# Performance work log

Measured on AMD Instinct MI355X. Metric: run time of the kernel, lower is better.

The kernel has to match this reference:

```python
import jax, jax.numpy as jnp
import numpy as np


def setup_inputs() -> dict:
    key = jax.random.key(0)
    k1, k2 = jax.random.split(key)
    z = jax.random.normal(k1, (16, 128, 32, 32), dtype=jnp.float32)
    e = jax.random.normal(k2, (8192, 128), dtype=jnp.float32)
    log_sigma = jnp.zeros((1,), dtype=jnp.float32)  # init_log_sigma = 0.0
    return {"z": z, "e": e, "log_sigma": log_sigma}


def reference(z, e, log_sigma):
    # z: [B, C, H, W] latents; e: [M, C] codebook; log_sigma: [1]
    B, C, H, W = z.shape
    zf = jnp.transpose(z, (0, 2, 3, 1)).reshape(-1, C)  # [N, C]
    N = zf.shape[0]
    M = e.shape[0]
    T = 1.0  # latent_temp default

    # squared L2 distance via expanded dot products: ||z||^2 + ||e||^2 - 2 z.e
    z_sq = jnp.sum(zf * zf, axis=1, keepdims=True)          # [N, 1]
    e_sq = jnp.sum(e * e, axis=1)[None, :]                  # [1, M]
    dist = jnp.maximum(z_sq + e_sq - 2.0 * (zf @ e.T), 0.0)  # [N, M]

    alpha = -1.0 / (2.0 * jnp.exp(log_sigma[0]) ** 2)
    A = alpha * dist / T                                     # [N, M]

    # np.log(np.e) == 1.0 in the original
    const = 0.5 * C * (2.0 * log_sigma - 1.0)                # [1]
    lse1_loss = -jnp.mean(T * jax.nn.logsumexp(A, axis=1)) + const + jnp.log(float(M))
    lse2_loss = -jnp.mean(T * jax.nn.logsumexp(A, axis=0)) + const + jnp.log(float(N))
    return lse1_loss, lse2_loss
```

## Files before the change

kernel.cpp:

```cpp
#include <hip/hip_runtime.h>
#include <hip/hip_bf16.h>

typedef unsigned short u16;
typedef __attribute__((ext_vector_type(8))) short short8;
typedef __attribute__((ext_vector_type(4))) float float4v;

#define N_ROWS 16384
#define M_COLS 8192
#define KDIM   128
#define SHIFT  64.0f
#define STRIPES 64
#define SPLITS  8
#define TILES   16

__device__ inline u16 f2bf(float f) {
  unsigned u = __builtin_bit_cast(unsigned, f);
  unsigned r = (u + 0x7fffu + ((u >> 16) & 1u)) >> 16;
  return (u16)r;
}

__global__ void prep(const float* __restrict__ z, const float* __restrict__ e,
                     u16* __restrict__ zf, u16* __restrict__ ef,
                     float* __restrict__ zsq, float* __restrict__ esq) {
  if (blockIdx.x < 512) {
    const int b = blockIdx.x >> 5, h = blockIdx.x & 31;
    __shared__ float tile[128 * 33];
    __shared__ float psum[8][32];
    const float* src = z + ((size_t)b * 128 * 32 + h) * 32;
    for (int idx = threadIdx.x; idx < 4096; idx += 256) {
      int c = idx >> 5, w = idx & 31;
      tile[c * 33 + w] = src[c * 1024 + w];
    }
    __syncthreads();
    {
      int w = threadIdx.x & 31, cg = threadIdx.x >> 5;
      float s = 0.f;
#pragma unroll
      for (int cc = 0; cc < 16; ++cc) {
        float v = tile[(cg * 16 + cc) * 33 + w];
        s = fmaf(v, v, s);
      }
      psum[cg][w] = s;
    }
    for (int idx = threadIdx.x; idx < 512; idx += 256) {
      int w = idx >> 4, g = idx & 15;
      short8 v;
#pragma unroll
      for (int cc = 0; cc < 8; ++cc) v[cc] = (short)f2bf(tile[(g * 8 + cc) * 33 + w]);
      *(short8*)&zf[((size_t)b * 1024 + h * 32 + w) * 128 + g * 8] = v;
    }
    __syncthreads();
    if (threadIdx.x < 32) {
      int w = threadIdx.x;
      float s = 0.f;
#pragma unroll
      for (int cg = 0; cg < 8; ++cg) s += psum[cg][w];
      zsq[b * 1024 + h * 32 + w] = s;
    }
  } else {
    const int gw = ((blockIdx.x - 512) * 256 + threadIdx.x) >> 6;
    const int ln = threadIdx.x & 63;
    for (int r = gw; r < M_COLS; r += 256) {
      float2 v = *(const float2*)&e[r * 128 + ln * 2];
      unsigned pk = (unsigned)f2bf(v.x) | ((unsigned)f2bf(v.y) << 16);
      *(unsigned*)&ef[r * 128 + ln * 2] = pk;
      float s = fmaf(v.x, v.x, v.y * v.y);
#pragma unroll
      for (int sh = 1; sh < 64; sh <<= 1) s += __shfl_xor(s, sh);
      if (ln == 0) esq[r] = s;
    }
  }
}

__global__ __launch_bounds__(256, 2) void gemm_lse(
    const u16* __restrict__ zf, const u16* __restrict__ ef,
    const float* __restrict__ zsq, const float* __restrict__ esq,
    const float* __restrict__ log_sigma,
    float* __restrict__ rpart, float* __restrict__ cpart) {
  __shared__ __align__(16) u16 et[2][64 * 128];
  __shared__ float colacc[1024];
  const int tid = threadIdx.x;
  const int ln = tid & 63, wv = tid >> 6;
  const int l15 = ln & 15, q = ln >> 4;
  const int stripe = blockIdx.x, split = blockIdx.y;
  const int colbase = split * 1024;

  for (int i = tid; i < 1024; i += 256) colacc[i] = 0.f;

  short8 af[4][4];
#pragma unroll
  for (int i = 0; i < 4; ++i)
#pragma unroll
    for (int kk = 0; kk < 4; ++kk)
      af[i][kk] = *(const short8*)(zf +
          (size_t)(stripe * 256 + wv * 64 + i * 16 + l15) * 128 + kk * 32 + q * 8);

  const float lsv = log_sigma[0];
  const float sg = __expf(lsv);
  const float alpha = -0.5f / (sg * sg);
  const float L2E = 1.44269504088896f;
  const float ca = alpha * L2E, cb = SHIFT * L2E, m2ca = -2.0f * ca;

  float4v zbl[4];
#pragma unroll
  for (int i = 0; i < 4; ++i) {
    float4v zs = *(const float4v*)(zsq + stripe * 256 + wv * 64 + i * 16 + q * 4);
#pragma unroll
    for (int r = 0; r < 4; ++r) zbl[i][r] = fmaf(ca, zs[r], cb);
  }

  float2 rs2[4][2];
#pragma unroll
  for (int i = 0; i < 4; ++i)
#pragma unroll
    for (int p = 0; p < 2; ++p) rs2[i][p] = make_float2(0.f, 0.f);

#define STAGE(tt)                                                              \
  do {                                                                         \
    const u16* efb = ef + (size_t)(colbase + (tt) * 64) * 128;                 \
    u16* dstb = et[(tt) & 1];                                                  \
    _Pragma("unroll")                                                          \
    for (int it = 0; it < 4; ++it) {                                           \
      int u = it * 256 + tid;                                                  \
      int r = u >> 4, p_ = u & 15;                                             \
      int g = p_ ^ (r & 15);                                                   \
      __builtin_amdgcn_global_load_lds(                                        \
          (const __attribute__((address_space(1))) unsigned int*)(efb + r * 128 + g * 8), \
          (__attribute__((address_space(3))) unsigned int*)(dstb + (it * 256 + wv * 64) * 8), \
          16, 0, 0);                                                           \
    }                                                                          \
  } while (0)

  STAGE(0);

  for (int t = 0; t < TILES; ++t) {
    __syncthreads();
    const u16* bb = et[t & 1];

    float4v acc[4][4];
#pragma unroll
    for (int kk = 0; kk < 4; ++kk) {
      short8 bfr[4];
      const int poff = ((kk * 4 + q) ^ l15) * 8;
#pragma unroll
      for (int j = 0; j < 4; ++j)
        bfr[j] = *(const short8*)(bb + (j * 16 + l15) * 128 + poff);
      if (kk == 0) {
#pragma unroll
        for (int i = 0; i < 4; ++i)
#pragma unroll
          for (int j = 0; j < 4; ++j)
            acc[i][j] = __builtin_amdgcn_mfma_f32_16x16x32_bf16(
                af[i][0], bfr[j], (float4v){0.f, 0.f, 0.f, 0.f}, 0, 0, 0);
      } else {
#pragma unroll
        for (int i = 0; i < 4; ++i)
#pragma unroll
          for (int j = 0; j < 4; ++j)
            acc[i][j] = __builtin_amdgcn_mfma_f32_16x16x32_bf16(
                af[i][kk], bfr[j], acc[i][j], 0, 0, 0);
      }
    }

    if (t + 1 < TILES) STAGE(t + 1);

    float ebv[4];
#pragma unroll
    for (int j = 0; j < 4; ++j) ebv[j] = ca * esq[colbase + t * 64 + j * 16 + l15];

    float2 cs2[4];
#pragma unroll
    for (int j = 0; j < 4; ++j) cs2[j] = make_float2(0.f, 0.f);

#pragma unroll
    for (int i = 0; i < 4; ++i) {
#pragma unroll
      for (int j = 0; j < 4; ++j) {
        float e0 = __builtin_amdgcn_exp2f(fmaf(acc[i][j][0], m2ca, zbl[i][0] + ebv[j]));
        float e1 = __builtin_amdgcn_exp2f(fmaf(acc[i][j][1], m2ca, zbl[i][1] + ebv[j]));
        float e2 = __builtin_amdgcn_exp2f(fmaf(acc[i][j][2], m2ca, zbl[i][2] + ebv[j]));
        float e3 = __builtin_amdgcn_exp2f(fmaf(acc[i][j][3], m2ca, zbl[i][3] + ebv[j]));
        rs2[i][0].x += e0; rs2[i][0].y += e1;
        rs2[i][1].x += e2; rs2[i][1].y += e3;
        cs2[j].x += e0 + e2; cs2[j].y += e1 + e3;
      }
    }
#pragma unroll
    for (int j = 0; j < 4; ++j) {
      float c = cs2[j].x + cs2[j].y;
      c += __shfl_xor(c, 16);
      c += __shfl_xor(c, 32);
      if (q == 0) atomicAdd(&colacc[t * 64 + j * 16 + l15], c);
    }
  }

  __syncthreads();
  for (int i = tid; i < 1024; i += 256)
    cpart[(size_t)stripe * 8192 + colbase + i] = colacc[i];

#pragma unroll
  for (int i = 0; i < 4; ++i)
#pragma unroll
    for (int p = 0; p < 2; ++p)
      for (int s = 1; s < 16; s <<= 1) {
        rs2[i][p].x += __shfl_xor(rs2[i][p].x, s);
        rs2[i][p].y += __shfl_xor(rs2[i][p].y, s);
      }
  if (l15 == 0) {
#pragma unroll
    for (int i = 0; i < 4; ++i) {
      int rbase = (size_t)0 + stripe * 256 + wv * 64 + i * 16 + q * 4;
      rpart[(size_t)split * N_ROWS + rbase + 0] = rs2[i][0].x;
      rpart[(size_t)split * N_ROWS + rbase + 1] = rs2[i][0].y;
      rpart[(size_t)split * N_ROWS + rbase + 2] = rs2[i][1].x;
      rpart[(size_t)split * N_ROWS + rbase + 3] = rs2[i][1].y;
    }
  }
#undef STAGE
}

__global__ void fin1(const float* __restrict__ rpart, const float* __restrict__ cpart,
                     double* __restrict__ lpart) {
  const int tid = threadIdx.x, b = blockIdx.x;
  double v;
  if (b < 64) {
    int row = b * 256 + tid;
    float s = 0.f;
#pragma unroll
    for (int p = 0; p < SPLITS; ++p) s += rpart[(size_t)p * N_ROWS + row];
    v = (double)logf(s);
  } else {
    int col = (b - 64) * 256 + tid;
    float s = 0.f;
#pragma unroll
    for (int p = 0; p < STRIPES; ++p) s += cpart[(size_t)p * M_COLS + col];
    v = (double)logf(s);
  }
  __shared__ double red[256];
  red[tid] = v;
  __syncthreads();
  for (int s = 128; s > 0; s >>= 1) {
    if (tid < s) red[tid] += red[tid + s];
    __syncthreads();
  }
  if (tid == 0) lpart[b] = red[0];
}

__global__ void fin2(const double* __restrict__ lpart,
                     const float* __restrict__ log_sigma, float* __restrict__ out) {
  const int tid = threadIdx.x;
  float lsv = log_sigma[0];
  float cst = 0.5f * 128.0f * (2.0f * lsv - 1.0f);
  if (tid == 0) {
    double s = 0.0;
    for (int i = 0; i < 64; ++i) s += lpart[i];
    out[0] = (float)(-(s / N_ROWS - (double)SHIFT)) + cst + logf((float)M_COLS);
  } else if (tid == 1) {
    double s = 0.0;
    for (int i = 64; i < 96; ++i) s += lpart[i];
    out[1] = (float)(-(s / M_COLS - (double)SHIFT)) + cst + logf((float)N_ROWS);
  }
}

extern "C" void kernel_launch(void* const* d_in, const int* in_sizes, int n_in,
                              void* d_out, int out_size, void* d_ws, size_t ws_size,
                              hipStream_t stream) {
  const float* z  = (const float*)d_in[0];
  const float* e  = (const float*)d_in[1];
  const float* ls = (const float*)d_in[2];
  float* out = (float*)d_out;
  char* ws = (char*)d_ws;
  u16*   zf    = (u16*)ws;
  u16*   ef    = (u16*)(ws + (4u << 20));
  float* zsq   = (float*)(ws + (6u << 20));
  float* esq   = (float*)(ws + (6u << 20) + (64u << 10));
  float* rpart = (float*)(ws + (6u << 20) + (96u << 10));
  float* cpart = (float*)(ws + (6u << 20) + (608u << 10));
  double* lpart = (double*)(ws + (6u << 20) + (608u << 10) + (2u << 20));

  prep<<<dim3(576), dim3(256), 0, stream>>>(z, e, zf, ef, zsq, esq);
  gemm_lse<<<dim3(STRIPES, SPLITS), dim3(256), 0, stream>>>(zf, ef, zsq, esq, ls, rpart, cpart);
  fin1<<<dim3(96), dim3(256), 0, stream>>>(rpart, cpart, lpart);
  fin2<<<dim3(1), dim3(64), 0, stream>>>(lpart, ls, out);
}
```

Before: 151.7 us.

## Halve GEMM row stripe, raise occupancy, fuse finalize kernels with atomic ticket

The GEMM+LSE kernel now handles 128 rows per block instead of 256, giving 1024 blocks with launch bounds allowing 4 blocks per CU, so more waves are resident to hide latency. The esq load is hoisted ahead of the barrier. The two finalize kernels are merged into one, which accumulates through double atomics and a last-block ticket, removing a launch. The prep kernel gets more blocks for codebook conversion and zeroes the accumulators. In exchange, each codebook tile is now reused across half as many rows, so LDS and global traffic for codebook tiles double, and the column partial buffer grows to 128 stripes.

```diff
diff --git a/kernel.cpp b/kernel.cpp
--- a/kernel.cpp
+++ b/kernel.cpp
@@ -9,7 +9,7 @@
 #define M_COLS 8192
 #define KDIM   128
 #define SHIFT  64.0f
-#define STRIPES 64
+#define STRIPES 128
 #define SPLITS  8
 #define TILES   16
 
@@ -21,7 +21,8 @@
 
 __global__ void prep(const float* __restrict__ z, const float* __restrict__ e,
                      u16* __restrict__ zf, u16* __restrict__ ef,
-                     float* __restrict__ zsq, float* __restrict__ esq) {
+                     float* __restrict__ zsq, float* __restrict__ esq,
+                     double* __restrict__ dacc, unsigned* __restrict__ dcnt) {
   if (blockIdx.x < 512) {
     const int b = blockIdx.x >> 5, h = blockIdx.x & 31;
     __shared__ float tile[128 * 33];
@@ -58,9 +59,14 @@
       zsq[b * 1024 + h * 32 + w] = s;
     }
   } else {
+    if (blockIdx.x == 512 && threadIdx.x == 0) {
+      __hip_atomic_store(&dacc[0], 0.0, __ATOMIC_RELAXED, __HIP_MEMORY_SCOPE_AGENT);
+      __hip_atomic_store(&dacc[1], 0.0, __ATOMIC_RELAXED, __HIP_MEMORY_SCOPE_AGENT);
+      __hip_atomic_store(dcnt, 0u, __ATOMIC_RELAXED, __HIP_MEMORY_SCOPE_AGENT);
+    }
     const int gw = ((blockIdx.x - 512) * 256 + threadIdx.x) >> 6;
     const int ln = threadIdx.x & 63;
-    for (int r = gw; r < M_COLS; r += 256) {
+    for (int r = gw; r < M_COLS; r += 512) {
       float2 v = *(const float2*)&e[r * 128 + ln * 2];
       unsigned pk = (unsigned)f2bf(v.x) | ((unsigned)f2bf(v.y) << 16);
       *(unsigned*)&ef[r * 128 + ln * 2] = pk;
@@ -72,7 +78,7 @@
   }
 }
 
-__global__ __launch_bounds__(256, 2) void gemm_lse(
+__global__ __launch_bounds__(256, 4) void gemm_lse(
     const u16* __restrict__ zf, const u16* __restrict__ ef,
     const float* __restrict__ zsq, const float* __restrict__ esq,
     const float* __restrict__ log_sigma,
@@ -87,13 +93,13 @@
 
   for (int i = tid; i < 1024; i += 256) colacc[i] = 0.f;
 
-  short8 af[4][4];
-#pragma unroll
-  for (int i = 0; i < 4; ++i)
+  short8 af[2][4];
+#pragma unroll
+  for (int i = 0; i < 2; ++i)
 #pragma unroll
     for (int kk = 0; kk < 4; ++kk)
       af[i][kk] = *(const short8*)(zf +
-          (size_t)(stripe * 256 + wv * 64 + i * 16 + l15) * 128 + kk * 32 + q * 8);
+          (size_t)(stripe * 128 + wv * 32 + i * 16 + l15) * 128 + kk * 32 + q * 8);
 
   const float lsv = log_sigma[0];
   const float sg = __expf(lsv);
@@ -101,17 +107,17 @@
   const float L2E = 1.44269504088896f;
   const float ca = alpha * L2E, cb = SHIFT * L2E, m2ca = -2.0f * ca;
 
-  float4v zbl[4];
-#pragma unroll
-  for (int i = 0; i < 4; ++i) {
-    float4v zs = *(const float4v*)(zsq + stripe * 256 + wv * 64 + i * 16 + q * 4);
+  float4v zbl[2];
+#pragma unroll
+  for (int i = 0; i < 2; ++i) {
+    float4v zs = *(const float4v*)(zsq + stripe * 128 + wv * 32 + i * 16 + q * 4);
 #pragma unroll
     for (int r = 0; r < 4; ++r) zbl[i][r] = fmaf(ca, zs[r], cb);
   }
 
-  float2 rs2[4][2];
-#pragma unroll
-  for (int i = 0; i < 4; ++i)
+  float2 rs2[2][2];
+#pragma unroll
+  for (int i = 0; i < 2; ++i)
 #pragma unroll
     for (int p = 0; p < 2; ++p) rs2[i][p] = make_float2(0.f, 0.f);
 
@@ -134,10 +140,14 @@
   STAGE(0);
 
   for (int t = 0; t < TILES; ++t) {
+    float ebv[4];
+#pragma unroll
+    for (int j = 0; j < 4; ++j) ebv[j] = ca * esq[colbase + t * 64 + j * 16 + l15];
+
     __syncthreads();
     const u16* bb = et[t & 1];
 
-    float4v acc[4][4];
+    float4v acc[2][4];
 #pragma unroll
     for (int kk = 0; kk < 4; ++kk) {
       short8 bfr[4];
@@ -147,14 +157,14 @@
         bfr[j] = *(const short8*)(bb + (j * 16 + l15) * 128 + poff);
       if (kk == 0) {
 #pragma unroll
-        for (int i = 0; i < 4; ++i)
+        for (int i = 0; i < 2; ++i)
 #pragma unroll
           for (int j = 0; j < 4; ++j)
             acc[i][j] = __builtin_amdgcn_mfma_f32_16x16x32_bf16(
                 af[i][0], bfr[j], (float4v){0.f, 0.f, 0.f, 0.f}, 0, 0, 0);
       } else {
 #pragma unroll
-        for (int i = 0; i < 4; ++i)
+        for (int i = 0; i < 2; ++i)
 #pragma unroll
           for (int j = 0; j < 4; ++j)
             acc[i][j] = __builtin_amdgcn_mfma_f32_16x16x32_bf16(
@@ -164,16 +174,12 @@
 
     if (t + 1 < TILES) STAGE(t + 1);
 
-    float ebv[4];
-#pragma unroll
-    for (int j = 0; j < 4; ++j) ebv[j] = ca * esq[colbase + t * 64 + j * 16 + l15];
-
     float2 cs2[4];
 #pragma unroll
     for (int j = 0; j < 4; ++j) cs2[j] = make_float2(0.f, 0.f);
 
 #pragma unroll
-    for (int i = 0; i < 4; ++i) {
+    for (int i = 0; i < 2; ++i) {
 #pragma unroll
       for (int j = 0; j < 4; ++j) {
         float e0 = __builtin_amdgcn_exp2f(fmaf(acc[i][j][0], m2ca, zbl[i][0] + ebv[j]));
@@ -199,7 +205,7 @@
     cpart[(size_t)stripe * 8192 + colbase + i] = colacc[i];
 
 #pragma unroll
-  for (int i = 0; i < 4; ++i)
+  for (int i = 0; i < 2; ++i)
 #pragma unroll
     for (int p = 0; p < 2; ++p)
       for (int s = 1; s < 16; s <<= 1) {
@@ -208,8 +214,8 @@
       }
   if (l15 == 0) {
 #pragma unroll
-    for (int i = 0; i < 4; ++i) {
-      int rbase = (size_t)0 + stripe * 256 + wv * 64 + i * 16 + q * 4;
+    for (int i = 0; i < 2; ++i) {
+      int rbase = stripe * 128 + wv * 32 + i * 16 + q * 4;
       rpart[(size_t)split * N_ROWS + rbase + 0] = rs2[i][0].x;
       rpart[(size_t)split * N_ROWS + rbase + 1] = rs2[i][0].y;
       rpart[(size_t)split * N_ROWS + rbase + 2] = rs2[i][1].x;
@@ -219,8 +225,10 @@
 #undef STAGE
 }
 
-__global__ void fin1(const float* __restrict__ rpart, const float* __restrict__ cpart,
-                     double* __restrict__ lpart) {
+__global__ void fin(const float* __restrict__ rpart, const float* __restrict__ cpart,
+                    const float* __restrict__ log_sigma,
+                    double* __restrict__ dacc, unsigned* __restrict__ dcnt,
+                    float* __restrict__ out) {
   const int tid = threadIdx.x, b = blockIdx.x;
   double v;
   if (b < 64) {
@@ -243,22 +251,18 @@
     if (tid < s) red[tid] += red[tid + s];
     __syncthreads();
   }
-  if (tid == 0) lpart[b] = red[0];
-}
-
-__global__ void fin2(const double* __restrict__ lpart,
-                     const float* __restrict__ log_sigma, float* __restrict__ out) {
-  const int tid = threadIdx.x;
-  float lsv = log_sigma[0];
-  float cst = 0.5f * 128.0f * (2.0f * lsv - 1.0f);
   if (tid == 0) {
-    double s = 0.0;
-    for (int i = 0; i < 64; ++i) s += lpart[i];
-    out[0] = (float)(-(s / N_ROWS - (double)SHIFT)) + cst + logf((float)M_COLS);
-  } else if (tid == 1) {
-    double s = 0.0;
-    for (int i = 64; i < 96; ++i) s += lpart[i];
-    out[1] = (float)(-(s / M_COLS - (double)SHIFT)) + cst + logf((float)N_ROWS);
+    atomicAdd(&dacc[b < 64 ? 0 : 1], red[0]);
+    __threadfence();
+    unsigned ticket = atomicAdd(dcnt, 1u);
+    if (ticket == 95u) {
+      double s1 = atomicAdd(&dacc[0], 0.0);
+      double s2 = atomicAdd(&dacc[1], 0.0);
+      float lsv = log_sigma[0];
+      float cst = 0.5f * 128.0f * (2.0f * lsv - 1.0f);
+      out[0] = (float)(-(s1 / N_ROWS - (double)SHIFT)) + cst + logf((float)M_COLS);
+      out[1] = (float)(-(s2 / M_COLS - (double)SHIFT)) + cst + logf((float)N_ROWS);
+    }
   }
 }
 
@@ -276,10 +280,10 @@
   float* esq   = (float*)(ws + (6u << 20) + (64u << 10));
   float* rpart = (float*)(ws + (6u << 20) + (96u << 10));
   float* cpart = (float*)(ws + (6u << 20) + (608u << 10));
-  double* lpart = (double*)(ws + (6u << 20) + (608u << 10) + (2u << 20));
-
-  prep<<<dim3(576), dim3(256), 0, stream>>>(z, e, zf, ef, zsq, esq);
+  double* dacc = (double*)(ws + (6u << 20) + (608u << 10) + (4u << 20));
+  unsigned* dcnt = (unsigned*)(ws + (6u << 20) + (608u << 10) + (4u << 20) + 16);
+
+  prep<<<dim3(640), dim3(256), 0, stream>>>(z, e, zf, ef, zsq, esq, dacc, dcnt);
   gemm_lse<<<dim3(STRIPES, SPLITS), dim3(256), 0, stream>>>(zf, ef, zsq, esq, ls, rpart, cpart);
-  fin1<<<dim3(96), dim3(256), 0, stream>>>(rpart, cpart, lpart);
-  fin2<<<dim3(1), dim3(64), 0, stream>>>(lpart, ls, out);
-}
+  fin<<<dim3(96), dim3(256), 0, stream>>>(rpart, cpart, ls, dacc, dcnt, out);
+}
```

Measured after the change: 161.9 us. 6.7% more time.
